# Kernel optimization log

Hardware: AMD Instinct MI355X
Metric: run time of the kernel (lower is better)

The kernel has to match this reference:

```python
import jax, jax.numpy as jnp
import numpy as np
from jax import lax

B, IN_CH, SKIP_CH, EMBED, H, W = 4, 256, 64, 64, 64, 64
RED = 8
QC = IN_CH // RED          # 32 q/k/v channels
GUIDE = 16.0
LN_EPS = 1e-5


def conv2d(x, w, b=None, groups=1):
    # x: [B,C,H,W], w: [O, C//groups, kh, kw], SAME padding, stride 1
    y = lax.conv_general_dilated(x, w, (1, 1), 'SAME',
                                 dimension_numbers=('NCHW', 'OIHW', 'NCHW'),
                                 feature_group_count=groups)
    return y if b is None else y + b[None, :, None, None]


def deform_conv(x, off, w, b):
    # torchvision DeformConv2d (DCNv1), 3x3, stride 1, pad 1
    # x: [B,C,H,W], off: [B,18,H,W] with (dy,dx) interleaved per kernel tap
    Bx, C, Hh, Ww = x.shape
    K = 9
    off = off.reshape(Bx, K, 2, Hh, Ww)
    gy, gx = jnp.meshgrid(jnp.arange(Hh, dtype=x.dtype),
                          jnp.arange(Ww, dtype=x.dtype), indexing='ij')
    kdy, kdx = jnp.meshgrid(jnp.arange(3, dtype=x.dtype) - 1,
                            jnp.arange(3, dtype=x.dtype) - 1, indexing='ij')
    py = gy[None, None] + kdy.reshape(K)[None, :, None, None] + off[:, :, 0]  # [B,K,H,W]
    px = gx[None, None] + kdx.reshape(K)[None, :, None, None] + off[:, :, 1]
    y0f = jnp.floor(py); x0f = jnp.floor(px)
    wy = py - y0f; wx = px - x0f
    y0 = y0f.astype(jnp.int32); x0 = x0f.astype(jnp.int32)

    def corner(yi, xi, wgt):
        valid = ((yi >= 0) & (yi < Hh) & (xi >= 0) & (xi < Ww)).astype(x.dtype)
        yc = jnp.clip(yi, 0, Hh - 1); xc = jnp.clip(xi, 0, Ww - 1)
        # per-batch gather -> [B, C, K, H, W]
        g = jax.vmap(lambda img, yy, xx: img[:, yy, xx])(x, yc, xc)
        return g * (wgt * valid)[:, None]

    vals = (corner(y0, x0, (1 - wy) * (1 - wx)) +
            corner(y0, x0 + 1, (1 - wy) * wx) +
            corner(y0 + 1, x0, wy * (1 - wx)) +
            corner(y0 + 1, x0 + 1, wy * wx))
    O = w.shape[0]
    return jnp.einsum('bckhw,ock->bohw', vals, w.reshape(O, C, K)) + b[None, :, None, None]


def setup_inputs() -> dict:
    key = jax.random.key(0)
    ks = jax.random.split(key, 16)
    rn = lambda k, s, sc=0.05: jax.random.normal(k, s, jnp.float32) * sc
    return {
        'x': jax.random.normal(ks[0], (B, IN_CH, H, W), jnp.float32),
        'skip': jax.random.normal(ks[1], (B, SKIP_CH, H // 2, W // 2), jnp.float32),
        'qkv_w': rn(ks[2], (3 * QC, IN_CH, 1, 1)), 'qkv_b': jnp.zeros((3 * QC,), jnp.float32),
        'proj_w': rn(ks[3], (IN_CH, QC, 1, 1)), 'proj_b': jnp.zeros((IN_CH,), jnp.float32),
        'edge_w': rn(ks[4], (SKIP_CH, 1, 3, 3)),
        'thick_w': rn(ks[5], (1, SKIP_CH, 1, 1)), 'thick_b': jnp.zeros((1,), jnp.float32),
        'off_w': rn(ks[6], (18, SKIP_CH, 3, 3), 0.02), 'off_b': jnp.zeros((18,), jnp.float32),
        'deform_w': rn(ks[7], (SKIP_CH, SKIP_CH, 3, 3)), 'deform_b': jnp.zeros((SKIP_CH,), jnp.float32),
        'ln_g': jnp.ones((EMBED,), jnp.float32), 'ln_b': jnp.zeros((EMBED,), jnp.float32),
        'mlp1_w': rn(ks[8], (4 * EMBED, EMBED, 1, 1)), 'mlp1_b': jnp.zeros((4 * EMBED,), jnp.float32),
        'dw_w': rn(ks[9], (4 * EMBED, 1, 3, 3)), 'dw_b': jnp.zeros((4 * EMBED,), jnp.float32),
        'mlp2_w': rn(ks[10], (EMBED, 4 * EMBED, 1, 1)), 'mlp2_b': jnp.zeros((EMBED,), jnp.float32),
        'down_w': rn(ks[11], (EMBED, IN_CH + SKIP_CH, 1, 1)), 'down_b': jnp.zeros((EMBED,), jnp.float32),
        'up_w': rn(ks[12], (IN_CH, EMBED, 1, 1)), 'up_b': jnp.zeros((IN_CH,), jnp.float32),
    }


def reference(x, skip, qkv_w, qkv_b, proj_w, proj_b, edge_w, thick_w, thick_b,
              off_w, off_b, deform_w, deform_b, ln_g, ln_b,
              mlp1_w, mlp1_b, dw_w, dw_b, mlp2_w, mlp2_b,
              down_w, down_b, up_w, up_b):
    Bx, C, Hh, Ww = x.shape
    # bilinear upsample (align_corners=False == half-pixel)
    skip_u = jax.image.resize(skip, (Bx, skip.shape[1], Hh, Ww), method='bilinear')

    # ---- EfficientCrossModalAttention ----
    qkv = conv2d(x, qkv_w, qkv_b)
    q, k, v = jnp.split(qkv, 3, axis=1)           # each [B, QC, H, W]
    c = q.shape[1]
    qf = q.reshape(Bx, c, Hh * Ww).transpose(0, 2, 1)   # [B, N, c]
    kf = k.reshape(Bx, c, Hh * Ww)                       # [B, c, N]
    vf = v.reshape(Bx, c, Hh * Ww).transpose(0, 2, 1)   # [B, N, c]
    attn = jax.nn.softmax(jnp.einsum('bnc,bcm->bnm', qf, kf) / jnp.sqrt(jnp.float32(c)), axis=-1)
    av = jnp.einsum('bnm,bmc->bnc', attn, vf).transpose(0, 2, 1).reshape(Bx, c, Hh, Ww)
    x2 = conv2d(av, proj_w, proj_b) + x

    # ---- edge / offset / deformable conv ----
    edge = conv2d(skip_u.mean(1, keepdims=True), edge_w)          # no bias
    thick = jax.nn.sigmoid(conv2d(skip_u, thick_w, thick_b))
    off = conv2d(edge, off_w, off_b) * (1.0 + GUIDE * thick)
    d = deform_conv(skip_u, off, deform_w, deform_b) + edge

    # ---- down -> TokenMixerBlock -> up ----
    e = conv2d(jnp.concatenate([x2, d], axis=1), down_w, down_b)  # [B, EMBED, H, W]
    h = e.transpose(0, 2, 3, 1)
    mu = h.mean(-1, keepdims=True)
    var = ((h - mu) ** 2).mean(-1, keepdims=True)
    h = (h - mu) / jnp.sqrt(var + LN_EPS) * ln_g + ln_b
    h = h.transpose(0, 3, 1, 2)
    h = jax.nn.gelu(conv2d(h, mlp1_w, mlp1_b), approximate=False)
    h = jax.nn.gelu(conv2d(h, dw_w, dw_b, groups=4 * EMBED), approximate=False)
    h = conv2d(h, mlp2_w, mlp2_b)
    t = h + e
    return conv2d(t, up_w, up_b)
```

## Files before the change

kernel.cpp:

```cpp
#include <hip/hip_runtime.h>
#include <hip/hip_bf16.h>
#include <math.h>

#define NB 4
#define NHW 4096
#define NBN (NB * NHW)

typedef const float* fp;
typedef unsigned short us;
typedef __attribute__((ext_vector_type(8))) short short8;
typedef __attribute__((ext_vector_type(4))) short short4v;
typedef __attribute__((ext_vector_type(4))) float floatx4;
typedef __attribute__((ext_vector_type(2))) unsigned int uint2v;
typedef __attribute__((ext_vector_type(4))) unsigned int uint4v;

__device__ __forceinline__ float b2f(__hip_bfloat16 v) { return __bfloat162float(v); }
__device__ __forceinline__ __hip_bfloat16 f2b(float v) { return __float2bfloat16(v); }
__device__ __forceinline__ us f2bu(float f) {
  __hip_bfloat16 h = __float2bfloat16(f);
  return *reinterpret_cast<us*>(&h);
}
__device__ __forceinline__ float bu2f(us u) {
  __hip_bfloat16 h = *reinterpret_cast<__hip_bfloat16*>(&u);
  return __bfloat162float(h);
}
__device__ __forceinline__ float gelu_ex(float x) { return 0.5f * x * (1.0f + erff(x * 0.70710678118654752f)); }
__device__ __forceinline__ short8 ld8(const us* p) { return *(const short8*)p; }

__global__ __launch_bounds__(256) void k_wq(fp qw, us* wq) {
  int i = blockIdx.x * 256 + threadIdx.x;
  if (i >= 96 * 256) return;
  wq[i] = f2bu(qw[i]);
}

__global__ __launch_bounds__(256) void k_wcast(fp pw, fp m1w, fp dnw, fp m2w, fp uw, fp dww,
                                               fp ew, fp ow, us* wc) {
  int i = blockIdx.x * 256 + threadIdx.x;
  if (i >= 99136) return;
  float v;
  if (i < 8192) v = pw[i];
  else if (i < 24576) v = m1w[i - 8192];
  else if (i < 45056) v = dnw[i - 24576];
  else if (i < 61440) v = m2w[i - 45056];
  else if (i < 77824) v = uw[i - 61440];
  else if (i < 80128) {
    int i2 = i - 77824;
    v = dww[(i2 & 255) * 9 + (i2 >> 8)];
  } else if (i < 80704) {
    int i2 = i - 80128;
    v = ew[(i2 & 63) * 9 + (i2 >> 6)];
  } else {
    int i2 = i - 80704;
    int oc = i2 / 576, rem = i2 % 576;
    int tap = rem >> 6, c = rem & 63;
    v = (oc < 18) ? ow[(oc * 64 + c) * 9 + tap] : 0.f;
  }
  wc[i] = f2bu(v);
}

__global__ __launch_bounds__(256) void k_wprep(fp dw, us* wbf) {
  int idx = blockIdx.x * 256 + threadIdx.x;
  if (idx >= 9 * 64 * 64) return;
  int c = idx & 63, oc = (idx >> 6) & 63, k = idx >> 12;
  wbf[idx] = f2bu(dw[(oc * 64 + c) * 9 + k]);
}

__global__ __launch_bounds__(256) void k_upsample(fp skip, float* su) {
  int idx = blockIdx.x * 256 + threadIdx.x;
  if (idx >= NB * 64 * NHW) return;
  int hw = idx & 4095, bc = idx >> 12;
  int y = hw >> 6, x = hw & 63;
  float fy = 0.5f * y - 0.25f, fx = 0.5f * x - 0.25f;
  float y0f = floorf(fy), x0f = floorf(fx);
  float wy = fy - y0f, wx = fx - x0f;
  int y0 = (int)y0f, x0 = (int)x0f;
  int y0c = min(31, max(0, y0)), y1c = min(31, max(0, y0 + 1));
  int x0c = min(31, max(0, x0)), x1c = min(31, max(0, x0 + 1));
  const float* p = skip + (size_t)bc * 1024;
  float v00 = p[y0c * 32 + x0c], v01 = p[y0c * 32 + x1c];
  float v10 = p[y1c * 32 + x0c], v11 = p[y1c * 32 + x1c];
  su[idx] = (1.f - wy) * ((1.f - wx) * v00 + wx * v01) + wy * ((1.f - wx) * v10 + wx * v11);
}

__global__ __launch_bounds__(256) void k_xpose(fp x, us* xT) {
  __shared__ float tile[64][65];
  int bid = blockIdx.x;
  int pt = bid & 63, ct = (bid >> 6) & 3, b = bid >> 8;
  int px0 = pt * 64, c0 = ct * 64;
  int tx = threadIdx.x & 63, ty = threadIdx.x >> 6;
  const float* src = x + ((size_t)(b * 256 + c0)) * NHW + px0;
#pragma unroll
  for (int i = 0; i < 16; i++) {
    int r = i * 4 + ty;
    tile[r][tx] = src[(size_t)r * NHW + tx];
  }
  __syncthreads();
  int cseg = threadIdx.x & 7, p0 = threadIdx.x >> 3;
#pragma unroll
  for (int h = 0; h < 2; h++) {
    int p = p0 + h * 32;
    short8 v;
#pragma unroll
    for (int j = 0; j < 8; j++) v[j] = (short)f2bu(tile[cseg * 8 + j][p]);
    *(short8*)&xT[((size_t)(b * NHW) + px0 + p) * 256 + c0 + cseg * 8] = v;
  }
}

__global__ __launch_bounds__(256) void k_qkv_g(const us* xT, const us* wq, fp bias, us* qkvb, us* kpx) {
  int wave = threadIdx.x >> 6, lane = threadIdx.x & 63;
  int quad = lane >> 4, l16 = lane & 15;
  int pxg0 = blockIdx.x * 64 + wave * 16;
  int b = pxg0 >> 12, hw0 = pxg0 & 4095;
  floatx4 acc[6];
#pragma unroll
  for (int m = 0; m < 6; m++) acc[m] = (floatx4){0.f, 0.f, 0.f, 0.f};
  const us* xrow = xT + (size_t)(pxg0 + l16) * 256 + quad * 8;
#pragma unroll
  for (int k0 = 0; k0 < 256; k0 += 32) {
    short8 bf = ld8(xrow + k0);
#pragma unroll
    for (int m = 0; m < 6; m++) {
      short8 af = ld8(wq + (size_t)(m * 16 + l16) * 256 + k0 + quad * 8);
      acc[m] = __builtin_amdgcn_mfma_f32_16x16x32_bf16(af, bf, acc[m], 0, 0, 0);
    }
  }
#pragma unroll
  for (int m = 0; m < 6; m++) {
    if (m == 2 || m == 3) {
      short4v pkv;
#pragma unroll
      for (int r = 0; r < 4; r++) {
        int oc = m * 16 + quad * 4 + r;
        pkv[r] = (short)f2bu(acc[m][r] + bias[oc]);
      }
      *(short4v*)&kpx[((size_t)(b * NHW) + hw0 + l16) * 32 + (m - 2) * 16 + quad * 4] = pkv;
    } else {
#pragma unroll
      for (int r = 0; r < 4; r++) {
        int oc = m * 16 + quad * 4 + r;
        float v = acc[m][r] + bias[oc];
        if (oc < 32) v *= 0.25503485f;
        qkvb[(size_t)(b * 96 + oc) * NHW + hw0 + l16] = f2bu(v);
      }
    }
  }
}

__global__ __launch_bounds__(256, 4) void k_attn(const us* qkvb, const us* kpx, us* Opart, float* ml) {
  int tid = threadIdx.x;
  int wave = tid >> 6, lane = tid & 63;
  int quad = lane >> 4, l16 = lane & 15;
  int blk = blockIdx.x;
  int kh = blk & 3;
  int rest = blk >> 2;
  int b = rest >> 6;
  int qbase = (rest & 63) * 64 + wave * 16;
  const us* qp = qkvb + (size_t)b * 96 * NHW;
  const us* vp = qp + 64 * NHW;
  const us* kb_base = kpx + (size_t)b * NHW * 32;

  short8 bq;
#pragma unroll
  for (int j = 0; j < 8; j++)
    bq[j] = (short)qp[(size_t)(quad * 8 + j) * NHW + qbase + l16];

  float m_r = -1e30f, l_r = 0.f;
  floatx4 o0 = {0.f, 0.f, 0.f, 0.f}, o1 = {0.f, 0.f, 0.f, 0.f};

  int kb0 = kh * 1024;
  short8 akf[8];
#pragma unroll
  for (int t = 0; t < 8; t++)
    akf[t] = ld8(kb_base + (size_t)(kb0 + t * 16 + l16) * 32 + quad * 8);

  for (int kb = kb0; kb < kb0 + 1024; kb += 128) {
    floatx4 sT[8];
    __builtin_amdgcn_s_setprio(1);
#pragma unroll
    for (int t = 0; t < 8; t++) {
      floatx4 z = {0.f, 0.f, 0.f, 0.f};
      sT[t] = __builtin_amdgcn_mfma_f32_16x16x32_bf16(akf[t], bq, z, 0, 0, 0);
    }
    __builtin_amdgcn_s_setprio(0);

    int kbn = (kb + 128 < kb0 + 1024) ? kb + 128 : kb0;
#pragma unroll
    for (int t = 0; t < 8; t++)
      akf[t] = ld8(kb_base + (size_t)(kbn + t * 16 + l16) * 32 + quad * 8);

    float mx = fmaxf(fmaxf(sT[0][0], sT[0][1]), fmaxf(sT[0][2], sT[0][3]));
#pragma unroll
    for (int t = 1; t < 8; t++)
      mx = fmaxf(mx, fmaxf(fmaxf(sT[t][0], sT[t][1]), fmaxf(sT[t][2], sT[t][3])));
    mx = fmaxf(mx, __shfl_xor(mx, 16));
    mx = fmaxf(mx, __shfl_xor(mx, 32));
    float mnew = fmaxf(m_r, mx);
    float alpha = exp2f(m_r - mnew);
    m_r = mnew;

    float rs = 0.f;
    unsigned pkw[8][2];
#pragma unroll
    for (int t = 0; t < 8; t++) {
      float p0 = exp2f(sT[t][0] - mnew);
      float p1 = exp2f(sT[t][1] - mnew);
      float p2 = exp2f(sT[t][2] - mnew);
      float p3 = exp2f(sT[t][3] - mnew);
      rs += (p0 + p1) + (p2 + p3);
      pkw[t][0] = (unsigned)f2bu(p0) | ((unsigned)f2bu(p1) << 16);
      pkw[t][1] = (unsigned)f2bu(p2) | ((unsigned)f2bu(p3) << 16);
    }
    rs += __shfl_xor(rs, 16);
    rs += __shfl_xor(rs, 32);
    l_r = l_r * alpha + rs;
#pragma unroll
    for (int r = 0; r < 4; r++) { o0[r] *= alpha; o1[r] *= alpha; }

    __builtin_amdgcn_s_setprio(1);
#pragma unroll
    for (int cc = 0; cc < 4; cc++) {
      uint2v t1 = __builtin_amdgcn_permlane32_swap(pkw[2 * cc][0], pkw[2 * cc + 1][0], false, false);
      uint2v t2 = __builtin_amdgcn_permlane16_swap(t1.x, t1.y, false, false);
      uint2v t3 = __builtin_amdgcn_permlane32_swap(pkw[2 * cc][1], pkw[2 * cc + 1][1], false, false);
      uint2v t4 = __builtin_amdgcn_permlane16_swap(t3.x, t3.y, false, false);
      uint4v pw = {t2.x, t4.x, t2.y, t4.y};
      short8 pa = *(short8*)&pw;
      short8 av0 = ld8(vp + (size_t)l16 * NHW + kb + cc * 32 + quad * 8);
      short8 av1 = ld8(vp + (size_t)(l16 + 16) * NHW + kb + cc * 32 + quad * 8);
      o0 = __builtin_amdgcn_mfma_f32_16x16x32_bf16(av0, pa, o0, 0, 0, 0);
      o1 = __builtin_amdgcn_mfma_f32_16x16x32_bf16(av1, pa, o1, 0, 0, 0);
    }
    __builtin_amdgcn_s_setprio(0);
  }

  int q = qbase + l16;
  size_t qg = (size_t)b * NHW + q;
  us* dst = Opart + ((size_t)kh * NBN + qg) * 32;
  short4v e0, e1;
#pragma unroll
  for (int r = 0; r < 4; r++) { e0[r] = (short)f2bu(o0[r]); e1[r] = (short)f2bu(o1[r]); }
  *(short4v*)(dst + quad * 4) = e0;
  *(short4v*)(dst + 16 + quad * 4) = e1;
  if (quad == 0) {
    ml[(size_t)kh * NBN + qg] = m_r;
    ml[(size_t)4 * NBN + (size_t)kh * NBN + qg] = l_r;
  }
}

__global__ __launch_bounds__(256) void k_merge(const us* Opart, const float* ml, us* avb) {
  int idx = blockIdx.x * 256 + threadIdx.x;
  int ch = idx & 31, qg = idx >> 5;
  float mk[4];
  float m = -1e30f;
#pragma unroll
  for (int kh = 0; kh < 4; kh++) { mk[kh] = ml[kh * NBN + qg]; m = fmaxf(m, mk[kh]); }
  float l = 0.f, v = 0.f;
#pragma unroll
  for (int kh = 0; kh < 4; kh++) {
    float a = exp2f(mk[kh] - m);
    l += ml[4 * NBN + kh * NBN + qg] * a;
    v += bu2f(Opart[((size_t)(kh * NBN) + qg) * 32 + ch]) * a;
  }
  avb[idx] = f2bu(v / l);
}

__global__ __launch_bounds__(256) void k_proj_g(const us* avb, const us* xT, const us* wpj, fp bias, us* x2T) {
  int wave = threadIdx.x >> 6, lane = threadIdx.x & 63;
  int quad = lane >> 4, l16 = lane & 15;
  int pxg0 = blockIdx.x * 64 + wave * 16;
  short8 act = ld8(avb + (size_t)(pxg0 + l16) * 32 + quad * 8);
  floatx4 acc[16];
#pragma unroll
  for (int n = 0; n < 16; n++) {
    short8 wf = ld8(wpj + (size_t)(n * 16 + l16) * 32 + quad * 8);
    floatx4 z = {0.f, 0.f, 0.f, 0.f};
    acc[n] = __builtin_amdgcn_mfma_f32_16x16x32_bf16(act, wf, z, 0, 0, 0);
  }
#pragma unroll
  for (int n = 0; n < 16; n++)
#pragma unroll
    for (int r = 0; r < 4; r++) {
      int px = pxg0 + quad * 4 + r;
      int oc = n * 16 + l16;
      size_t oidx = (size_t)px * 256 + oc;
      x2T[oidx] = f2bu(acc[n][r] + bias[oc] + bu2f(xT[oidx]));
    }
}

__global__ __launch_bounds__(256) void k_meanthick(const float* su, fp tw, fp tb, float* sm, float* thick) {
  int idx = blockIdx.x * 256 + threadIdx.x;
  if (idx >= NB * NHW) return;
  int hw = idx & 4095, b = idx >> 12;
  const float* p = su + (size_t)b * 64 * NHW + hw;
  float s = 0.f, ts = 0.f;
#pragma unroll 8
  for (int c = 0; c < 64; c++) {
    float v = p[(size_t)c * NHW];
    s += v;
    ts += v * tw[c];
  }
  sm[idx] = s * (1.f / 64.f);
  float z = ts + tb[0];
  thick[idx] = 1.f / (1.f + __expf(-z));
}

__global__ __launch_bounds__(256) void k_edge_px(const float* sm, const us* ewT, us* edgeT) {
  int idx = blockIdx.x * 256 + threadIdx.x;
  int cb = idx & 7, pxg = idx >> 3;
  int b = pxg >> 12, hw = pxg & 4095;
  int y = hw >> 6, x = hw & 63;
  int c0 = cb * 8;
  float acc[8] = {0.f, 0.f, 0.f, 0.f, 0.f, 0.f, 0.f, 0.f};
#pragma unroll
  for (int ky = 0; ky < 3; ky++) {
#pragma unroll
    for (int kx = 0; kx < 3; kx++) {
      int yy = y + ky - 1, xx = x + kx - 1;
      if (yy >= 0 && yy < 64 && xx >= 0 && xx < 64) {
        float sv = sm[b * NHW + yy * 64 + xx];
        short8 wv = ld8(ewT + (ky * 3 + kx) * 64 + c0);
#pragma unroll
        for (int j = 0; j < 8; j++) acc[j] += sv * bu2f((us)wv[j]);
      }
    }
  }
  short8 pk;
#pragma unroll
  for (int j = 0; j < 8; j++) pk[j] = (short)f2bu(acc[j]);
  *(short8*)(edgeT + (size_t)pxg * 64 + c0) = pk;
}

__global__ __launch_bounds__(256) void k_off_g(const us* edgeT, const us* woff, fp ob,
                                               const float* thick, float* offb) {
  int wave = threadIdx.x >> 6, lane = threadIdx.x & 63;
  int quad = lane >> 4, l16 = lane & 15;
  int pxg0 = blockIdx.x * 64 + wave * 16;
  int b = pxg0 >> 12;
  int pxl = pxg0 + l16;
  int hwl = pxl & 4095;
  int yl = hwl >> 6, xl = hwl & 63;
  floatx4 acc[2];
  acc[0] = (floatx4){0.f, 0.f, 0.f, 0.f};
  acc[1] = (floatx4){0.f, 0.f, 0.f, 0.f};
  const short8 zz = {0, 0, 0, 0, 0, 0, 0, 0};
#pragma unroll
  for (int t = 0; t < 9; t++) {
    int yy = yl + t / 3 - 1, xx = xl + t % 3 - 1;
    bool valid = (yy >= 0 && yy < 64 && xx >= 0 && xx < 64);
    const us* arow = edgeT + ((size_t)(b * NHW + yy * 64 + xx)) * 64;
#pragma unroll
    for (int s = 0; s < 2; s++) {
      short8 act = valid ? ld8(arow + s * 32 + quad * 8) : zz;
      int kk = t * 64 + s * 32 + quad * 8;
#pragma unroll
      for (int n = 0; n < 2; n++) {
        short8 wf = ld8(woff + (size_t)(n * 16 + l16) * 576 + kk);
        acc[n] = __builtin_amdgcn_mfma_f32_16x16x32_bf16(act, wf, acc[n], 0, 0, 0);
      }
    }
  }
#pragma unroll
  for (int n = 0; n < 2; n++)
#pragma unroll
    for (int r = 0; r < 4; r++) {
      int oc = n * 16 + l16;
      if (oc < 18) {
        int px = pxg0 + quad * 4 + r;
        int hw = px & 4095;
        float v = (acc[n][r] + ob[oc]) * (1.f + 16.f * thick[px]);
        offb[(size_t)(b * 18 + oc) * NHW + hw] = v;
      }
    }
}

__global__ __launch_bounds__(256) void k_deform(const float* su, const float* offb,
                                                const us* wbf, fp db,
                                                const us* edgeT, us* dbufT) {
  __shared__ __align__(16) us samT[4][16][72];
  int tid = threadIdx.x;
  int wave = tid >> 6, lane = tid & 63;
  int quad = lane >> 4, l16 = lane & 15;
  int b = blockIdx.x >> 6, row = blockIdx.x & 63;
  const float* sub = su + (size_t)b * 64 * NHW;

  int sp = lane & 15, sq = lane >> 4;
  int hw_s = row * 64 + wave * 16 + sp;
  int x_s = wave * 16 + sp;

  floatx4 acc[4];
#pragma unroll
  for (int a = 0; a < 4; a++) acc[a] = (floatx4){0.f, 0.f, 0.f, 0.f};

  for (int k = 0; k < 9; k++) {
    float dy = offb[((size_t)(b * 18 + 2 * k)) * NHW + hw_s];
    float dx = offb[((size_t)(b * 18 + 2 * k + 1)) * NHW + hw_s];
    float py = (float)(row + k / 3 - 1) + dy;
    float pxf = (float)(x_s + k % 3 - 1) + dx;
    float y0f = floorf(py), x0f = floorf(pxf);
    float wy = py - y0f, wx = pxf - x0f;
    int y0 = (int)y0f, x0 = (int)x0f;
    int y1 = y0 + 1, x1 = x0 + 1;
    float vy0 = (y0 >= 0 && y0 < 64) ? 1.f : 0.f;
    float vy1 = (y1 >= 0 && y1 < 64) ? 1.f : 0.f;
    float vx0 = (x0 >= 0 && x0 < 64) ? 1.f : 0.f;
    float vx1 = (x1 >= 0 && x1 < 64) ? 1.f : 0.f;
    float w00 = (1.f - wy) * (1.f - wx) * vy0 * vx0;
    float w01 = (1.f - wy) * wx * vy0 * vx1;
    float w10 = wy * (1.f - wx) * vy1 * vx0;
    float w11 = wy * wx * vy1 * vx1;
    int y0c = min(63, max(0, y0)), y1c = min(63, max(0, y1));
    int x0c = min(63, max(0, x0)), x1c = min(63, max(0, x1));
    int i00 = y0c * 64 + x0c, i01 = y0c * 64 + x1c;
    int i10 = y1c * 64 + x0c, i11 = y1c * 64 + x1c;

#pragma unroll
    for (int i = 0; i < 16; i += 2) {
      int c0 = sq * 16 + i;
      const float* s0 = sub + (size_t)c0 * NHW;
      const float* s1 = s0 + NHW;
      float v0 = w00 * s0[i00] + w01 * s0[i01] + w10 * s0[i10] + w11 * s0[i11];
      float v1 = w00 * s1[i00] + w01 * s1[i01] + w10 * s1[i10] + w11 * s1[i11];
      unsigned int pk = (unsigned int)f2bu(v0) | ((unsigned int)f2bu(v1) << 16);
      *(unsigned int*)&samT[wave][sp][c0] = pk;
    }

#pragma unroll
    for (int s = 0; s < 2; s++) {
      short8 bfrag = *(const short8*)&samT[wave][l16][s * 32 + quad * 8];
#pragma unroll
      for (int a = 0; a < 4; a++) {
        short8 afrag = ld8(wbf + ((size_t)(k * 64 + a * 16 + l16) * 64 + s * 32 + quad * 8));
        acc[a] = __builtin_amdgcn_mfma_f32_16x16x32_bf16(bfrag, afrag, acc[a], 0, 0, 0);
      }
    }
  }

#pragma unroll
  for (int a = 0; a < 4; a++)
#pragma unroll
    for (int r = 0; r < 4; r++) {
      int oc = a * 16 + l16;
      int pxr = row * 64 + wave * 16 + quad * 4 + r;
      size_t rowi = (size_t)(b * NHW) + pxr;
      float v = acc[a][r] + db[oc] + bu2f(edgeT[rowi * 64 + oc]);
      dbufT[rowi * 64 + oc] = f2bu(v);
    }
}

__global__ __launch_bounds__(256) void k_down_g(const us* x2T, const us* dbufT, const us* wd, fp bias, float* ebufT) {
  int wave = threadIdx.x >> 6, lane = threadIdx.x & 63;
  int quad = lane >> 4, l16 = lane & 15;
  int pxg0 = blockIdx.x * 64 + wave * 16;
  floatx4 acc[4];
#pragma unroll
  for (int m = 0; m < 4; m++) acc[m] = (floatx4){0.f, 0.f, 0.f, 0.f};
  const us* xrow = x2T + (size_t)(pxg0 + l16) * 256 + quad * 8;
#pragma unroll
  for (int k0 = 0; k0 < 256; k0 += 32) {
    short8 act = ld8(xrow + k0);
#pragma unroll
    for (int m = 0; m < 4; m++) {
      short8 wf = ld8(wd + (size_t)(m * 16 + l16) * 320 + k0 + quad * 8);
      acc[m] = __builtin_amdgcn_mfma_f32_16x16x32_bf16(act, wf, acc[m], 0, 0, 0);
    }
  }
  const us* drow = dbufT + (size_t)(pxg0 + l16) * 64 + quad * 8;
#pragma unroll
  for (int k0 = 0; k0 < 64; k0 += 32) {
    short8 act = ld8(drow + k0);
#pragma unroll
    for (int m = 0; m < 4; m++) {
      short8 wf = ld8(wd + (size_t)(m * 16 + l16) * 320 + 256 + k0 + quad * 8);
      acc[m] = __builtin_amdgcn_mfma_f32_16x16x32_bf16(act, wf, acc[m], 0, 0, 0);
    }
  }
#pragma unroll
  for (int m = 0; m < 4; m++)
#pragma unroll
    for (int r = 0; r < 4; r++) {
      int px = pxg0 + quad * 4 + r;
      int oc = m * 16 + l16;
      ebufT[(size_t)px * 64 + oc] = acc[m][r] + bias[oc];
    }
}

__global__ __launch_bounds__(256) void k_ln(const float* eT, fp g, fp bt, us* hnT) {
  int idx = blockIdx.x * 256 + threadIdx.x;
  if (idx >= NB * NHW) return;
  const float* p = eT + (size_t)idx * 64;
  float v[64];
  float s = 0.f;
#pragma unroll
  for (int i = 0; i < 16; i++) {
    float4 t = ((const float4*)p)[i];
    v[i * 4] = t.x; v[i * 4 + 1] = t.y; v[i * 4 + 2] = t.z; v[i * 4 + 3] = t.w;
    s += t.x + t.y + t.z + t.w;
  }
  float mu = s * (1.f / 64.f);
  float q = 0.f;
#pragma unroll
  for (int c = 0; c < 64; c++) { float d = v[c] - mu; q += d * d; }
  float rstd = rsqrtf(q * (1.f / 64.f) + 1e-5f);
  us* o = hnT + (size_t)idx * 64;
#pragma unroll
  for (int j = 0; j < 8; j++) {
    short8 pk;
#pragma unroll
    for (int t = 0; t < 8; t++) {
      int c = j * 8 + t;
      pk[t] = (short)f2bu((v[c] - mu) * rstd * g[c] + bt[c]);
    }
    *(short8*)(o + j * 8) = pk;
  }
}

__global__ __launch_bounds__(256) void k_mlp1_g(const us* hnT, const us* wm1, fp bias, us* h1T) {
  int wave = threadIdx.x >> 6, lane = threadIdx.x & 63;
  int quad = lane >> 4, l16 = lane & 15;
  int pxg0 = blockIdx.x * 64 + wave * 16;
  floatx4 acc[16];
#pragma unroll
  for (int m = 0; m < 16; m++) acc[m] = (floatx4){0.f, 0.f, 0.f, 0.f};
  const us* hrow = hnT + (size_t)(pxg0 + l16) * 64 + quad * 8;
#pragma unroll
  for (int k0 = 0; k0 < 64; k0 += 32) {
    short8 act = ld8(hrow + k0);
#pragma unroll
    for (int m = 0; m < 16; m++) {
      short8 wf = ld8(wm1 + (size_t)(m * 16 + l16) * 64 + k0 + quad * 8);
      acc[m] = __builtin_amdgcn_mfma_f32_16x16x32_bf16(act, wf, acc[m], 0, 0, 0);
    }
  }
#pragma unroll
  for (int m = 0; m < 16; m++)
#pragma unroll
    for (int r = 0; r < 4; r++) {
      int px = pxg0 + quad * 4 + r;
      int oc = m * 16 + l16;
      h1T[(size_t)px * 256 + oc] = f2bu(gelu_ex(acc[m][r] + bias[oc]));
    }
}

__global__ __launch_bounds__(256) void k_dw(const us* h1T, const us* wdwT, fp bias, us* h2T) {
  int idx = blockIdx.x * 256 + threadIdx.x;
  int cb = idx & 31, pxg = idx >> 5;
  int b = pxg >> 12, hw = pxg & 4095;
  int y = hw >> 6, x = hw & 63;
  int c0 = cb * 8;
  float4 b0 = *(const float4*)(bias + c0);
  float4 b1 = *(const float4*)(bias + c0 + 4);
  float acc[8] = {b0.x, b0.y, b0.z, b0.w, b1.x, b1.y, b1.z, b1.w};
#pragma unroll
  for (int ky = 0; ky < 3; ky++) {
#pragma unroll
    for (int kx = 0; kx < 3; kx++) {
      int tap = ky * 3 + kx;
      short8 wv = ld8(wdwT + tap * 256 + c0);
      int yy = y + ky - 1, xx = x + kx - 1;
      if (yy >= 0 && yy < 64 && xx >= 0 && xx < 64) {
        short8 vv = ld8(h1T + ((size_t)(b * NHW + yy * 64 + xx)) * 256 + c0);
#pragma unroll
        for (int j = 0; j < 8; j++)
          acc[j] += bu2f((us)vv[j]) * bu2f((us)wv[j]);
      }
    }
  }
  short8 pk;
#pragma unroll
  for (int j = 0; j < 8; j++) pk[j] = (short)f2bu(gelu_ex(acc[j]));
  *(short8*)(h2T + (size_t)pxg * 256 + c0) = pk;
}

__global__ __launch_bounds__(256) void k_mlp2_g(const us* h2T, const us* wm2, fp bias, const float* ebufT, us* tbufT) {
  int wave = threadIdx.x >> 6, lane = threadIdx.x & 63;
  int quad = lane >> 4, l16 = lane & 15;
  int pxg0 = blockIdx.x * 64 + wave * 16;
  floatx4 acc[4];
#pragma unroll
  for (int m = 0; m < 4; m++) acc[m] = (floatx4){0.f, 0.f, 0.f, 0.f};
  const us* hrow = h2T + (size_t)(pxg0 + l16) * 256 + quad * 8;
#pragma unroll
  for (int k0 = 0; k0 < 256; k0 += 32) {
    short8 act = ld8(hrow + k0);
#pragma unroll
    for (int m = 0; m < 4; m++) {
      short8 wf = ld8(wm2 + (size_t)(m * 16 + l16) * 256 + k0 + quad * 8);
      acc[m] = __builtin_amdgcn_mfma_f32_16x16x32_bf16(act, wf, acc[m], 0, 0, 0);
    }
  }
#pragma unroll
  for (int m = 0; m < 4; m++)
#pragma unroll
    for (int r = 0; r < 4; r++) {
      int px = pxg0 + quad * 4 + r;
      int oc = m * 16 + l16;
      size_t oidx = (size_t)px * 64 + oc;
      tbufT[oidx] = f2bu(acc[m][r] + bias[oc] + ebufT[oidx]);
    }
}

__global__ __launch_bounds__(256) void k_up_g(const us* tbufT, const us* wu, fp bias, float* out) {
  int wave = threadIdx.x >> 6, lane = threadIdx.x & 63;
  int quad = lane >> 4, l16 = lane & 15;
  int pxg0 = blockIdx.x * 64 + wave * 16;
  int b = pxg0 >> 12, hw0 = pxg0 & 4095;
  floatx4 acc[16];
#pragma unroll
  for (int m = 0; m < 16; m++) acc[m] = (floatx4){0.f, 0.f, 0.f, 0.f};
  const us* trow = tbufT + (size_t)(pxg0 + l16) * 64 + quad * 8;
#pragma unroll
  for (int k0 = 0; k0 < 64; k0 += 32) {
    short8 bf = ld8(trow + k0);
#pragma unroll
    for (int m = 0; m < 16; m++) {
      short8 af = ld8(wu + (size_t)(m * 16 + l16) * 64 + k0 + quad * 8);
      acc[m] = __builtin_amdgcn_mfma_f32_16x16x32_bf16(af, bf, acc[m], 0, 0, 0);
    }
  }
#pragma unroll
  for (int m = 0; m < 16; m++)
#pragma unroll
    for (int r = 0; r < 4; r++) {
      int oc = m * 16 + quad * 4 + r;
      out[(size_t)(b * 256 + oc) * NHW + hw0 + l16] = acc[m][r] + bias[oc];
    }
}

extern "C" void kernel_launch(void* const* d_in, const int* in_sizes, int n_in,
                              void* d_out, int out_size, void* d_ws, size_t ws_size,
                              hipStream_t stream) {
  fp x = (fp)d_in[0], skip = (fp)d_in[1], qkv_w = (fp)d_in[2], qkv_b = (fp)d_in[3],
     proj_w = (fp)d_in[4], proj_b = (fp)d_in[5], edge_w = (fp)d_in[6], thick_w = (fp)d_in[7],
     thick_b = (fp)d_in[8], off_w = (fp)d_in[9], off_b = (fp)d_in[10], deform_w = (fp)d_in[11],
     deform_b = (fp)d_in[12], ln_g = (fp)d_in[13], ln_b = (fp)d_in[14], mlp1_w = (fp)d_in[15],
     mlp1_b = (fp)d_in[16], dw_w = (fp)d_in[17], dw_b = (fp)d_in[18], mlp2_w = (fp)d_in[19],
     mlp2_b = (fp)d_in[20], down_w = (fp)d_in[21], down_b = (fp)d_in[22], up_w = (fp)d_in[23],
     up_b = (fp)d_in[24];

  float* ws = (float*)d_ws;
  float* su    = ws + 0;
  us* qkvb  = (us*)(ws + 1048576);
  us* avb   = (us*)(ws + 1835008);
  us* wc    = (us*)(ws + 2097152);
  float* ml = ws + 2146720;
  us* kpx   = (us*)(ws + 2277792);
  us* x2T   = (us*)(ws + 3145728);
  us* edgeT = (us*)(ws + 5242880);
  float* offb  = ws + 6291456;
  float* sm    = ws + 6586368;
  float* thick = ws + 6602752;
  us* dbufT = (us*)(ws + 6619136);
  float* ebufT = ws + 7143424;
  us* xT   = x2T;
  us* wq   = dbufT;
  us* wbf  = (us*)sm;
  us* Opart = (us*)ebufT;
  us* hnT  = qkvb;
  us* h1T  = x2T;
  us* h2T  = (us*)ws;
  us* tbufT = edgeT;

  dim3 blk(256);
  k_wq<<<96, blk, 0, stream>>>(qkv_w, wq);
  k_wcast<<<388, blk, 0, stream>>>(proj_w, mlp1_w, down_w, mlp2_w, up_w, dw_w, edge_w, off_w, wc);
  k_upsample<<<(NB * 64 * NHW) / 256, blk, 0, stream>>>(skip, su);
  k_xpose<<<1024, blk, 0, stream>>>(x, xT);
  k_qkv_g<<<(NB * NHW) / 64, blk, 0, stream>>>(xT, wq, qkv_b, qkvb, kpx);
  k_attn<<<(NB * NHW) / 16, blk, 0, stream>>>(qkvb, kpx, Opart, ml);
  k_merge<<<(NB * NHW * 32) / 256, blk, 0, stream>>>(Opart, ml, avb);
  k_proj_g<<<(NB * NHW) / 64, blk, 0, stream>>>(avb, xT, wc, proj_b, x2T);
  k_meanthick<<<(NB * NHW) / 256, blk, 0, stream>>>(su, thick_w, thick_b, sm, thick);
  k_edge_px<<<(NB * NHW * 8) / 256, blk, 0, stream>>>(sm, wc + 80128, edgeT);
  k_off_g<<<(NB * NHW) / 64, blk, 0, stream>>>(edgeT, wc + 80704, off_b, thick, offb);
  k_wprep<<<144, blk, 0, stream>>>(deform_w, wbf);
  k_deform<<<NB * 64, blk, 0, stream>>>(su, offb, wbf, deform_b, edgeT, dbufT);
  k_down_g<<<(NB * NHW) / 64, blk, 0, stream>>>(x2T, dbufT, wc + 24576, down_b, ebufT);
  k_ln<<<(NB * NHW) / 256, blk, 0, stream>>>(ebufT, ln_g, ln_b, hnT);
  k_mlp1_g<<<(NB * NHW) / 64, blk, 0, stream>>>(hnT, wc + 8192, mlp1_b, h1T);
  k_dw<<<(NB * NHW * 32) / 256, blk, 0, stream>>>(h1T, wc + 77824, dw_b, h2T);
  k_mlp2_g<<<(NB * NHW) / 64, blk, 0, stream>>>(h2T, wc + 45056, mlp2_b, ebufT, tbufT);
  k_up_g<<<(NB * NHW) / 64, blk, 0, stream>>>(tbufT, wc + 61440, up_b, (float*)d_out);
}
```

Baseline: 316.6 us.

## Split attention keys eight ways and use permlane reductions with packed bf16 converts

The attention kernel now splits the key range into eight chunks of 512 instead of four of 1024. This doubles the block count and raises the occupancy hint so more waves hide latency. Row max and sum reductions use permlane swaps instead of shuffles, and probabilities are packed with a single v_cvt_pk_bf16 instruction. The merge kernel combines eight partials, which adds merge traffic, and the workspace buffers are moved to make room for the larger partial and stats arrays.

```diff
diff --git a/kernel.cpp b/kernel.cpp
--- a/kernel.cpp
+++ b/kernel.cpp
@@ -5,6 +5,7 @@
 #define NB 4
 #define NHW 4096
 #define NBN (NB * NHW)
+#define KSPLIT 8
 
 typedef const float* fp;
 typedef unsigned short us;
@@ -26,6 +27,24 @@
 }
 __device__ __forceinline__ float gelu_ex(float x) { return 0.5f * x * (1.0f + erff(x * 0.70710678118654752f)); }
 __device__ __forceinline__ short8 ld8(const us* p) { return *(const short8*)p; }
+
+__device__ __forceinline__ unsigned cvt_pk_bf16(float lo, float hi) {
+  unsigned r;
+  asm("v_cvt_pk_bf16_f32 %0, %1, %2" : "=v"(r) : "v"(lo), "v"(hi));
+  return r;
+}
+__device__ __forceinline__ float qmax4(float v) {
+  uint2v p = __builtin_amdgcn_permlane16_swap(__float_as_uint(v), __float_as_uint(v), false, false);
+  v = fmaxf(__uint_as_float(p.x), __uint_as_float(p.y));
+  p = __builtin_amdgcn_permlane32_swap(__float_as_uint(v), __float_as_uint(v), false, false);
+  return fmaxf(__uint_as_float(p.x), __uint_as_float(p.y));
+}
+__device__ __forceinline__ float qsum4(float v) {
+  uint2v p = __builtin_amdgcn_permlane16_swap(__float_as_uint(v), __float_as_uint(v), false, false);
+  v = __uint_as_float(p.x) + __uint_as_float(p.y);
+  p = __builtin_amdgcn_permlane32_swap(__float_as_uint(v), __float_as_uint(v), false, false);
+  return __uint_as_float(p.x) + __uint_as_float(p.y);
+}
 
 __global__ __launch_bounds__(256) void k_wq(fp qw, us* wq) {
   int i = blockIdx.x * 256 + threadIdx.x;
@@ -146,13 +165,13 @@
   }
 }
 
-__global__ __launch_bounds__(256, 4) void k_attn(const us* qkvb, const us* kpx, us* Opart, float* ml) {
+__global__ __launch_bounds__(256, 8) void k_attn(const us* qkvb, const us* kpx, us* Opart, float* ml) {
   int tid = threadIdx.x;
   int wave = tid >> 6, lane = tid & 63;
   int quad = lane >> 4, l16 = lane & 15;
   int blk = blockIdx.x;
-  int kh = blk & 3;
-  int rest = blk >> 2;
+  int kh = blk & 7;
+  int rest = blk >> 3;
   int b = rest >> 6;
   int qbase = (rest & 63) * 64 + wave * 16;
   const us* qp = qkvb + (size_t)b * 96 * NHW;
@@ -167,13 +186,13 @@
   float m_r = -1e30f, l_r = 0.f;
   floatx4 o0 = {0.f, 0.f, 0.f, 0.f}, o1 = {0.f, 0.f, 0.f, 0.f};
 
-  int kb0 = kh * 1024;
+  int kb0 = kh * 512;
   short8 akf[8];
 #pragma unroll
   for (int t = 0; t < 8; t++)
     akf[t] = ld8(kb_base + (size_t)(kb0 + t * 16 + l16) * 32 + quad * 8);
 
-  for (int kb = kb0; kb < kb0 + 1024; kb += 128) {
+  for (int kb = kb0; kb < kb0 + 512; kb += 128) {
     floatx4 sT[8];
     __builtin_amdgcn_s_setprio(1);
 #pragma unroll
@@ -183,22 +202,23 @@
     }
     __builtin_amdgcn_s_setprio(0);
 
-    int kbn = (kb + 128 < kb0 + 1024) ? kb + 128 : kb0;
+    int kbn = (kb + 128 < kb0 + 512) ? kb + 128 : kb0;
 #pragma unroll
     for (int t = 0; t < 8; t++)
       akf[t] = ld8(kb_base + (size_t)(kbn + t * 16 + l16) * 32 + quad * 8);
 
-    float mx = fmaxf(fmaxf(sT[0][0], sT[0][1]), fmaxf(sT[0][2], sT[0][3]));
-#pragma unroll
-    for (int t = 1; t < 8; t++)
-      mx = fmaxf(mx, fmaxf(fmaxf(sT[t][0], sT[t][1]), fmaxf(sT[t][2], sT[t][3])));
-    mx = fmaxf(mx, __shfl_xor(mx, 16));
-    mx = fmaxf(mx, __shfl_xor(mx, 32));
+    float tm[8];
+#pragma unroll
+    for (int t = 0; t < 8; t++)
+      tm[t] = fmaxf(fmaxf(fmaxf(sT[t][0], sT[t][1]), sT[t][2]), sT[t][3]);
+    float mx = fmaxf(fmaxf(fmaxf(tm[0], tm[1]), tm[2]), tm[3]);
+    mx = fmaxf(fmaxf(fmaxf(fmaxf(mx, tm[4]), tm[5]), tm[6]), tm[7]);
+    mx = qmax4(mx);
     float mnew = fmaxf(m_r, mx);
     float alpha = exp2f(m_r - mnew);
     m_r = mnew;
 
-    float rs = 0.f;
+    float rs0 = 0.f, rs1 = 0.f;
     unsigned pkw[8][2];
 #pragma unroll
     for (int t = 0; t < 8; t++) {
@@ -206,12 +226,12 @@
       float p1 = exp2f(sT[t][1] - mnew);
       float p2 = exp2f(sT[t][2] - mnew);
       float p3 = exp2f(sT[t][3] - mnew);
-      rs += (p0 + p1) + (p2 + p3);
-      pkw[t][0] = (unsigned)f2bu(p0) | ((unsigned)f2bu(p1) << 16);
-      pkw[t][1] = (unsigned)f2bu(p2) | ((unsigned)f2bu(p3) << 16);
-    }
-    rs += __shfl_xor(rs, 16);
-    rs += __shfl_xor(rs, 32);
+      rs0 += p0 + p1;
+      rs1 += p2 + p3;
+      pkw[t][0] = cvt_pk_bf16(p0, p1);
+      pkw[t][1] = cvt_pk_bf16(p2, p3);
+    }
+    float rs = qsum4(rs0 + rs1);
     l_r = l_r * alpha + rs;
 #pragma unroll
     for (int r = 0; r < 4; r++) { o0[r] *= alpha; o1[r] *= alpha; }
@@ -243,22 +263,22 @@
   *(short4v*)(dst + 16 + quad * 4) = e1;
   if (quad == 0) {
     ml[(size_t)kh * NBN + qg] = m_r;
-    ml[(size_t)4 * NBN + (size_t)kh * NBN + qg] = l_r;
+    ml[(size_t)KSPLIT * NBN + (size_t)kh * NBN + qg] = l_r;
   }
 }
 
 __global__ __launch_bounds__(256) void k_merge(const us* Opart, const float* ml, us* avb) {
   int idx = blockIdx.x * 256 + threadIdx.x;
   int ch = idx & 31, qg = idx >> 5;
-  float mk[4];
+  float mk[KSPLIT];
   float m = -1e30f;
 #pragma unroll
-  for (int kh = 0; kh < 4; kh++) { mk[kh] = ml[kh * NBN + qg]; m = fmaxf(m, mk[kh]); }
+  for (int kh = 0; kh < KSPLIT; kh++) { mk[kh] = ml[kh * NBN + qg]; m = fmaxf(m, mk[kh]); }
   float l = 0.f, v = 0.f;
 #pragma unroll
-  for (int kh = 0; kh < 4; kh++) {
+  for (int kh = 0; kh < KSPLIT; kh++) {
     float a = exp2f(mk[kh] - m);
-    l += ml[4 * NBN + kh * NBN + qg] * a;
+    l += ml[KSPLIT * NBN + kh * NBN + qg] * a;
     v += bu2f(Opart[((size_t)(kh * NBN) + qg) * 32 + ch]) * a;
   }
   avb[idx] = f2bu(v / l);
@@ -643,7 +663,7 @@
   us* avb   = (us*)(ws + 1835008);
   us* wc    = (us*)(ws + 2097152);
   float* ml = ws + 2146720;
-  us* kpx   = (us*)(ws + 2277792);
+  us* kpx   = (us*)(ws + 2408864);
   us* x2T   = (us*)(ws + 3145728);
   us* edgeT = (us*)(ws + 5242880);
   float* offb  = ws + 6291456;
@@ -654,7 +674,7 @@
   us* xT   = x2T;
   us* wq   = dbufT;
   us* wbf  = (us*)sm;
-  us* Opart = (us*)ebufT;
+  us* Opart = (us*)(ws + 5242880);
   us* hnT  = qkvb;
   us* h1T  = x2T;
   us* h2T  = (us*)ws;
@@ -666,7 +686,7 @@
   k_upsample<<<(NB * 64 * NHW) / 256, blk, 0, stream>>>(skip, su);
   k_xpose<<<1024, blk, 0, stream>>>(x, xT);
   k_qkv_g<<<(NB * NHW) / 64, blk, 0, stream>>>(xT, wq, qkv_b, qkvb, kpx);
-  k_attn<<<(NB * NHW) / 16, blk, 0, stream>>>(qkvb, kpx, Opart, ml);
+  k_attn<<<(NB * NHW / 64) * KSPLIT, blk, 0, stream>>>(qkvb, kpx, Opart, ml);
   k_merge<<<(NB * NHW * 32) / 256, blk, 0, stream>>>(Opart, ml, avb);
   k_proj_g<<<(NB * NHW) / 64, blk, 0, stream>>>(avb, xT, wc, proj_b, x2T);
   k_meanthick<<<(NB * NHW) / 256, blk, 0, stream>>>(su, thick_w, thick_b, sm, thick);
```

New measurement: 369.6 us. +16.7%, slower.
